# Kernel optimization log

Hardware: AMD Instinct MI355X
Metric: run time of the kernel (lower is better)

The kernel has to match this reference:

```python
import jax, jax.numpy as jnp
import numpy as np
from itertools import permutations

B, Nm, S, K, H, OUT = 32, 128, 16, 4, 128, 1
LG, LI, LGL = 3, 2, 2  # num_layer, num_layer_id, num_layer_global
EPS = 1e-5


def _ln(x, g, b):
    m = jnp.mean(x, -1, keepdims=True)
    v = jnp.mean(jnp.square(x - m), -1, keepdims=True)
    return (x - m) * jax.lax.rsqrt(v + EPS) * g + b


def _block(x, W1, b1, W2, b2, g, bn):
    # Linear -> ReLU -> Linear -> LayerNorm -> ReLU
    h = jax.nn.relu(x @ W1 + b1)
    return jax.nn.relu(_ln(h @ W2 + b2, g, bn))


def setup_inputs() -> dict:
    key = jax.random.key(0)
    ks = iter(jax.random.split(key, 64))
    nrm = lambda shape, s=0.05: jax.random.normal(next(ks), shape, jnp.float32) * s
    x = nrm((B, Nm, 1), 1.0)
    adj = (jax.random.uniform(next(ks), (B, Nm, Nm)) < 0.05).astype(jnp.float32)
    # allperm: all permutations of [1..K-1] with 0 prepended, transposed -> (K, permdim)
    ap = np.array(list(permutations(range(1, K))), dtype=np.int32)
    ap = np.concatenate([np.zeros((ap.shape[0], 1), np.int32), ap], axis=1).T
    allperm = jnp.asarray(ap)
    Ssub = B * S
    base = jax.random.randint(next(ks), (Ssub,), 0, Nm - K)
    subgs = base[:, None] + jnp.arange(K, dtype=jnp.int32)[None, :]  # distinct nodes per subgraph
    num_subg = jnp.full((B,), S, jnp.int32)
    num_node = jnp.full((B,), Nm, jnp.int32)
    d = dict(x=x, adj=adj,
             idemb=nrm((K + 2, H)),
             in_W1=nrm((1, H)), in_b1=jnp.zeros((H,)), in_W2=nrm((H, H)), in_b2=jnp.zeros((H,)),
             in_g=jnp.ones((H,)), in_bn=jnp.zeros((H,)),
             gW1=nrm((LG, H, H)), gb1=jnp.zeros((LG, H)), gW2=nrm((LG, H, H)), gb2=jnp.zeros((LG, H)),
             gg=jnp.ones((LG, H)), gbn=jnp.zeros((LG, H)),
             iW1=nrm((LI, H, H)), ib1=jnp.zeros((LI, H)), iW2=nrm((LI, H, H)), ib2=jnp.zeros((LI, H)),
             ig=jnp.ones((LI, H)), ibn=jnp.zeros((LI, H)),
             glW1=nrm((LGL, H, H)), glb1=jnp.zeros((LGL, H)), glW2=nrm((LGL, H, H)), glb2=jnp.zeros((LGL, H)),
             glg=jnp.ones((LGL, H)), glbn=jnp.zeros((LGL, H)),
             s1_W=nrm((H, H)), s1_b=jnp.zeros((H,)), s2_W=nrm((H, H)), s2_b=jnp.zeros((H,)),
             rW1=nrm((H, H)), rb1=jnp.zeros((H,)), rW2=nrm((H, H)), rb2=jnp.zeros((H,)),
             rg=jnp.ones((H,)), rbn=jnp.zeros((H,)),
             out_W=nrm((H, OUT)), out_b=jnp.zeros((OUT,)),
             subgs=subgs, num_subg=num_subg, num_node=num_node, allperm=allperm)
    return d


def reference(x, adj, idemb, in_W1, in_b1, in_W2, in_b2, in_g, in_bn,
              gW1, gb1, gW2, gb2, gg, gbn,
              iW1, ib1, iW2, ib2, ig, ibn,
              glW1, glb1, glW2, glb2, glg, glbn,
              s1_W, s1_b, s2_W, s2_b,
              rW1, rb1, rW2, rb2, rg, rbn,
              out_W, out_b, subgs, num_subg, num_node, allperm):
    Bsz, N = x.shape[0], x.shape[1]
    Ssub, k = subgs.shape
    permdim = allperm.shape[1]
    # input embedding MLP
    h = _block(x, in_W1, in_b1, in_W2, in_b2, in_g, in_bn)  # (B, Nm, H)
    Hd = h.shape[-1]
    # subgraph -> graph batch map (ns_b = S per graph; Ssub static)
    subgbatch = jnp.repeat(jnp.arange(Bsz), num_subg, total_repeat_length=Ssub)
    # identity labeling: z starts as ones, labeled nodes get idemb(allperm[pos])
    lb = jnp.repeat(jnp.arange(Ssub), k)          # label batch (subgraph idx)
    lnodes = subgs.reshape(-1)                    # node ids within graph
    ni = jnp.tile(jnp.arange(k), Ssub)            # position within subgraph
    vals = idemb[allperm[ni]]                     # (Ssub*k, permdim, H)
    z = jnp.ones((Ssub, N, permdim, Hd), x.dtype)
    z = z.at[lb, lnodes].multiply(vals)
    # graph message passing on full graphs
    for l in range(gW1.shape[0]):
        m = jnp.einsum('bij,bjd->bid', adj, h)
        h = h + _block(m, gW1[l], gb1[l], gW2[l], gb2[l], gg[l], gbn[l])
    hs = h[subgbatch]        # (Ssub, Nm, H)
    sadj = adj[subgbatch]    # (Ssub, Nm, Nm)
    # id message passing over permutation channels
    for l in range(iW1.shape[0]):
        m = jnp.einsum('bij,bjpd->bipd', sadj, z)
        z = z + _block(m, iW1[l], ib1[l], iW2[l], ib2[l], ig[l], ibn[l])
    # zero out padded (null) nodes
    null_mask = jnp.arange(N)[None, :] >= num_node[:, None]  # (B, Nm)
    z = jnp.where(null_mask[subgbatch][:, :, None, None], 0.0, z)
    z = jax.nn.relu(z.mean(axis=2) @ s1_W + s1_b)  # setmlp1, (Ssub, Nm, H)
    hs = hs + z
    for l in range(glW1.shape[0]):
        m = jnp.einsum('bij,bjd->bid', sadj, hs)
        hs = hs + _block(m, glW1[l], glb1[l], glW2[l], glb2[l], glg[l], glbn[l])
    hs = jax.nn.relu(hs.sum(axis=1) @ s2_W + s2_b)  # setmlp2, (Ssub, H)
    pooled = jax.ops.segment_max(hs, subgbatch, num_segments=Bsz)  # global max pool
    pooled = pooled + _block(pooled, rW1, rb1, rW2, rb2, rg, rbn)  # setmlp3 (1 layer)
    return pooled @ out_W + out_b  # (B, OUT)
```

## Files before the change

kernel.cpp:

```cpp
#include <hip/hip_runtime.h>
#include <hip/hip_bf16.h>
#include <string.h>

typedef __hip_bfloat16 bf16;
typedef short v8s __attribute__((ext_vector_type(8)));
typedef float v4f __attribute__((ext_vector_type(4)));

#define H_ 128
#define P_ 6
#define K_ 4

__device__ __forceinline__ float s2f(short s) {
    unsigned int u = ((unsigned int)(unsigned short)s) << 16;
    float f; __builtin_memcpy(&f, &u, 4); return f;
}
__device__ __forceinline__ short f2s(float v) {
    bf16 h = __float2bfloat16(v);
    short s; __builtin_memcpy(&s, &h, 2); return s;
}
__device__ __forceinline__ v4f MFMA(v8s a, v8s b, v4f c) {
    return __builtin_amdgcn_mfma_f32_16x16x32_bf16(a, b, c, 0, 0, 0);
}

__global__ __launch_bounds__(128) void k_deg(const float* __restrict__ adj, float* __restrict__ degf)
{
    __shared__ float red[128];
    const int row = blockIdx.x, t = threadIdx.x;
    red[t] = adj[(size_t)row * 128 + t];
    __syncthreads();
    for (int s = 64; s > 0; s >>= 1) {
        if (t < s) red[t] += red[t + s];
        __syncthreads();
    }
    if (t == 0) degf[row] = red[0];
}

__global__ __launch_bounds__(128) void k_adjb(const float* __restrict__ adj, bf16* __restrict__ adjb)
{
    const size_t i = (size_t)blockIdx.x * 128 + threadIdx.x;
    adjb[i] = __float2bfloat16(adj[i]);
}

__global__ __launch_bounds__(128) void k_wt8(
    const float* s0, const float* s1, const float* s2, const float* s3,
    const float* s4, const float* s5, const float* s6, const float* s7,
    bf16* __restrict__ dst)
{
    const int w = blockIdx.x >> 7, n = blockIdx.x & 127, k = threadIdx.x;
    const float* arr[8] = {s0, s1, s2, s3, s4, s5, s6, s7};
    dst[(size_t)w * 16384 + n * 128 + k] = __float2bfloat16(arr[w][k * 128 + n]);
}

__global__ __launch_bounds__(128) void k_wt1(const float* __restrict__ src, bf16* __restrict__ dst)
{
    const int n = blockIdx.x, k = threadIdx.x;
    dst[n * 128 + k] = __float2bfloat16(src[k * 128 + n]);
}

__global__ __launch_bounds__(256) void k_h_fused(
    const float* __restrict__ x, const bf16* __restrict__ adjb,
    const float* __restrict__ inW1, const float* __restrict__ inb1,
    const bf16* __restrict__ inW2t, const float* __restrict__ inb2,
    const float* __restrict__ ing, const float* __restrict__ inbn,
    const bf16* __restrict__ WTg,
    const float* __restrict__ gb1, const float* __restrict__ gb2,
    const float* __restrict__ gg, const float* __restrict__ gbn,
    float* __restrict__ hb)
{
    __shared__ __align__(16) short sHsT[128][136];
    __shared__ __align__(16) short sM[128][136];
    __shared__ float sP[15][128];
    const int t = threadIdx.x;
    const int g = blockIdx.x;
    const int wave = t >> 6, lane = t & 63, quad = lane >> 4, l16 = lane & 15;
    const int wrow = wave << 5;

    for (int u = t; u < 15 * 128; u += 256) {
        const int a = u >> 7, n = u & 127;
        const float* src;
        if (a == 0) src = inb2;
        else if (a == 1) src = ing;
        else if (a == 2) src = inbn;
        else {
            const int l = (a - 3) >> 2, pp = (a - 3) & 3;
            src = (pp == 0) ? gb1 + l * 128 : (pp == 1) ? gb2 + l * 128
                : (pp == 2) ? gg + l * 128 : gbn + l * 128;
        }
        sP[a][n] = src[n];
    }

    v8s aA[2][4];
    {
        const bf16* ar = adjb + (size_t)g * 16384;
        #pragma unroll
        for (int mt = 0; mt < 2; ++mt)
            #pragma unroll
            for (int kk = 0; kk < 4; ++kk)
                aA[mt][kk] = *(const v8s*)(ar + (size_t)(wrow + mt * 16 + l16) * 128 + kk * 32 + quad * 8);
    }

    {
        const int i = t >> 1, half = (t & 1) * 64;
        const float xv = x[(size_t)g * 128 + i];
        #pragma unroll
        for (int fb = 0; fb < 64; fb += 8) {
            v8s pk;
            #pragma unroll
            for (int e = 0; e < 8; ++e)
                pk[e] = f2s(fmaxf(fmaf(xv, inW1[half + fb + e], inb1[half + fb + e]), 0.f));
            *(v8s*)&sM[i][half + fb] = pk;
        }
    }
    __syncthreads();

    v4f acc[2][8];
    #pragma unroll
    for (int mt = 0; mt < 2; ++mt)
        #pragma unroll
        for (int nt = 0; nt < 8; ++nt) acc[mt][nt] = (v4f){0.f, 0.f, 0.f, 0.f};
    #pragma unroll
    for (int kk = 0; kk < 4; ++kk) {
        v8s a0 = *(const v8s*)&sM[wrow + l16][kk * 32 + quad * 8];
        v8s a1 = *(const v8s*)&sM[wrow + 16 + l16][kk * 32 + quad * 8];
        #pragma unroll
        for (int nt = 0; nt < 8; ++nt) {
            v8s b = *(const v8s*)(inW2t + (nt * 16 + l16) * 128 + kk * 32 + quad * 8);
            acc[0][nt] = MFMA(a0, b, acc[0][nt]);
            acc[1][nt] = MFMA(a1, b, acc[1][nt]);
        }
    }
    float hs_reg[2][8][4];
    #pragma unroll
    for (int mt = 0; mt < 2; ++mt)
        #pragma unroll
        for (int r = 0; r < 4; ++r) {
            float s = 0.f, qq = 0.f;
            #pragma unroll
            for (int nt = 0; nt < 8; ++nt) {
                float u = acc[mt][nt][r] + sP[0][nt * 16 + l16];
                acc[mt][nt][r] = u;
                s += u; qq += u * u;
            }
            #pragma unroll
            for (int d = 1; d < 16; d <<= 1) {
                s += __shfl_xor(s, d);
                qq += __shfl_xor(qq, d);
            }
            float mn = s * (1.f / 128.f);
            float rs = rsqrtf(qq * (1.f / 128.f) - mn * mn + 1e-5f);
            const int i = wrow + mt * 16 + quad * 4 + r;
            #pragma unroll
            for (int nt = 0; nt < 8; ++nt) {
                const int n = nt * 16 + l16;
                float v = fmaxf((acc[mt][nt][r] - mn) * rs * sP[1][n] + sP[2][n], 0.f);
                hs_reg[mt][nt][r] = v;
                sHsT[n][i] = f2s(v);
            }
        }
    __syncthreads();

    for (int l = 0; l < 3; ++l) {
        const bf16* W1t = WTg + (size_t)(2 * l) * 16384;
        const bf16* W2t = WTg + (size_t)(2 * l + 1) * 16384;
        #pragma unroll
        for (int mt = 0; mt < 2; ++mt)
            #pragma unroll
            for (int nt = 0; nt < 8; ++nt) acc[mt][nt] = (v4f){0.f, 0.f, 0.f, 0.f};
        #pragma unroll
        for (int kk = 0; kk < 4; ++kk)
            #pragma unroll
            for (int nt = 0; nt < 8; ++nt) {
                v8s b = *(const v8s*)&sHsT[nt * 16 + l16][kk * 32 + quad * 8];
                acc[0][nt] = MFMA(aA[0][kk], b, acc[0][nt]);
                acc[1][nt] = MFMA(aA[1][kk], b, acc[1][nt]);
            }
        #pragma unroll
        for (int nt = 0; nt < 8; ++nt)
            #pragma unroll
            for (int mt = 0; mt < 2; ++mt)
                #pragma unroll
                for (int r = 0; r < 4; ++r)
                    sM[wrow + mt * 16 + quad * 4 + r][nt * 16 + l16] = f2s(acc[mt][nt][r]);
        __syncthreads();
        #pragma unroll
        for (int mt = 0; mt < 2; ++mt)
            #pragma unroll
            for (int nt = 0; nt < 8; ++nt) acc[mt][nt] = (v4f){0.f, 0.f, 0.f, 0.f};
        #pragma unroll
        for (int kk = 0; kk < 4; ++kk) {
            v8s a0 = *(const v8s*)&sM[wrow + l16][kk * 32 + quad * 8];
            v8s a1 = *(const v8s*)&sM[wrow + 16 + l16][kk * 32 + quad * 8];
            #pragma unroll
            for (int nt = 0; nt < 8; ++nt) {
                v8s b = *(const v8s*)(W1t + (nt * 16 + l16) * 128 + kk * 32 + quad * 8);
                acc[0][nt] = MFMA(a0, b, acc[0][nt]);
                acc[1][nt] = MFMA(a1, b, acc[1][nt]);
            }
        }
        #pragma unroll
        for (int nt = 0; nt < 8; ++nt) {
            float bb = sP[3 + 4 * l + 0][nt * 16 + l16];
            #pragma unroll
            for (int mt = 0; mt < 2; ++mt)
                #pragma unroll
                for (int r = 0; r < 4; ++r)
                    sM[wrow + mt * 16 + quad * 4 + r][nt * 16 + l16] = f2s(fmaxf(acc[mt][nt][r] + bb, 0.f));
        }
        #pragma unroll
        for (int mt = 0; mt < 2; ++mt)
            #pragma unroll
            for (int nt = 0; nt < 8; ++nt) acc[mt][nt] = (v4f){0.f, 0.f, 0.f, 0.f};
        #pragma unroll
        for (int kk = 0; kk < 4; ++kk) {
            v8s a0 = *(const v8s*)&sM[wrow + l16][kk * 32 + quad * 8];
            v8s a1 = *(const v8s*)&sM[wrow + 16 + l16][kk * 32 + quad * 8];
            #pragma unroll
            for (int nt = 0; nt < 8; ++nt) {
                v8s b = *(const v8s*)(W2t + (nt * 16 + l16) * 128 + kk * 32 + quad * 8);
                acc[0][nt] = MFMA(a0, b, acc[0][nt]);
                acc[1][nt] = MFMA(a1, b, acc[1][nt]);
            }
        }
        #pragma unroll
        for (int mt = 0; mt < 2; ++mt)
            #pragma unroll
            for (int r = 0; r < 4; ++r) {
                float s = 0.f, qq = 0.f;
                #pragma unroll
                for (int nt = 0; nt < 8; ++nt) {
                    float u = acc[mt][nt][r] + sP[3 + 4 * l + 1][nt * 16 + l16];
                    acc[mt][nt][r] = u;
                    s += u; qq += u * u;
                }
                #pragma unroll
                for (int d = 1; d < 16; d <<= 1) {
                    s += __shfl_xor(s, d);
                    qq += __shfl_xor(qq, d);
                }
                float mn = s * (1.f / 128.f);
                float rs = rsqrtf(qq * (1.f / 128.f) - mn * mn + 1e-5f);
                const int i = wrow + mt * 16 + quad * 4 + r;
                #pragma unroll
                for (int nt = 0; nt < 8; ++nt) {
                    const int n = nt * 16 + l16;
                    float v = fmaxf((acc[mt][nt][r] - mn) * rs * sP[3 + 4 * l + 2][n] + sP[3 + 4 * l + 3][n], 0.f);
                    float h2 = hs_reg[mt][nt][r] + v;
                    hs_reg[mt][nt][r] = h2;
                    sHsT[n][i] = f2s(h2);
                }
            }
        __syncthreads();
    }

    #pragma unroll
    for (int mt = 0; mt < 2; ++mt)
        #pragma unroll
        for (int nt = 0; nt < 8; ++nt)
            #pragma unroll
            for (int r = 0; r < 4; ++r) {
                const int i = wrow + mt * 16 + quad * 4 + r;
                const int n = nt * 16 + l16;
                hb[((size_t)(g * 128 + i)) * 128 + n] = hs_reg[mt][nt][r];
            }
}

__global__ __launch_bounds__(256) void k_id1_fused(
    const float* __restrict__ adj, const float* __restrict__ degf,
    const int* __restrict__ subgs, const int* __restrict__ allperm,
    const float* __restrict__ idemb, bf16* __restrict__ outb,
    const bf16* __restrict__ W1t, const float* __restrict__ b1,
    const bf16* __restrict__ W2t, const float* __restrict__ b2,
    const float* __restrict__ gam, const float* __restrict__ bet)
{
    __shared__ __align__(16) short sB[128][136];
    __shared__ float sE[K_][128];
    const int t = threadIdx.x;
    const int bi = blockIdx.x;
    const int b_s = bi / 6, p = bi - b_s * 6;
    const int g = b_s >> 4;
    const int wave = t >> 6, lane = t & 63;
    const int quad = lane >> 4, l16 = lane & 15;
    const int wrow = wave << 5;

    int nodeq[K_];
    #pragma unroll
    for (int q = 0; q < K_; ++q) nodeq[q] = subgs[b_s * K_ + q];

    for (int u = t; u < K_ * 128; u += 256) {
        const int q = u >> 7, f = u & 127;
        sE[q][f] = idemb[(size_t)allperm[q * P_ + p] * H_ + f] - 1.f;
    }
    __syncthreads();

    {
        const int i = t >> 1, half = (t & 1) * 64;
        const int gi = g * 128 + i;
        const float dg = degf[gi];
        float aq[K_];
        #pragma unroll
        for (int q = 0; q < K_; ++q) aq[q] = adj[(size_t)gi * 128 + nodeq[q]];
        #pragma unroll
        for (int f = 0; f < 64; ++f) {
            float v = dg;
            #pragma unroll
            for (int q = 0; q < K_; ++q) v = fmaf(aq[q], sE[q][half + f], v);
            sB[i][half + f] = f2s(v);
        }
    }
    __syncthreads();

    v4f acc[2][8];
    #pragma unroll
    for (int mt = 0; mt < 2; ++mt)
        #pragma unroll
        for (int nt = 0; nt < 8; ++nt) acc[mt][nt] = (v4f){0.f, 0.f, 0.f, 0.f};
    #pragma unroll
    for (int kk = 0; kk < 4; ++kk) {
        v8s a0 = *(const v8s*)&sB[wrow + l16][kk * 32 + quad * 8];
        v8s a1 = *(const v8s*)&sB[wrow + 16 + l16][kk * 32 + quad * 8];
        #pragma unroll
        for (int nt = 0; nt < 8; ++nt) {
            v8s b = *(const v8s*)(W1t + (nt * 16 + l16) * 128 + kk * 32 + quad * 8);
            acc[0][nt] = MFMA(a0, b, acc[0][nt]);
            acc[1][nt] = MFMA(a1, b, acc[1][nt]);
        }
    }
    #pragma unroll
    for (int nt = 0; nt < 8; ++nt) {
        float bb = b1[nt * 16 + l16];
        #pragma unroll
        for (int mt = 0; mt < 2; ++mt)
            #pragma unroll
            for (int r = 0; r < 4; ++r)
                sB[wrow + mt * 16 + quad * 4 + r][nt * 16 + l16] = f2s(fmaxf(acc[mt][nt][r] + bb, 0.f));
    }
    #pragma unroll
    for (int mt = 0; mt < 2; ++mt)
        #pragma unroll
        for (int nt = 0; nt < 8; ++nt) acc[mt][nt] = (v4f){0.f, 0.f, 0.f, 0.f};
    #pragma unroll
    for (int kk = 0; kk < 4; ++kk) {
        v8s a0 = *(const v8s*)&sB[wrow + l16][kk * 32 + quad * 8];
        v8s a1 = *(const v8s*)&sB[wrow + 16 + l16][kk * 32 + quad * 8];
        #pragma unroll
        for (int nt = 0; nt < 8; ++nt) {
            v8s b = *(const v8s*)(W2t + (nt * 16 + l16) * 128 + kk * 32 + quad * 8);
            acc[0][nt] = MFMA(a0, b, acc[0][nt]);
            acc[1][nt] = MFMA(a1, b, acc[1][nt]);
        }
    }
    float bb2[8], gv[8], bv[8];
    #pragma unroll
    for (int nt = 0; nt < 8; ++nt) {
        int n = nt * 16 + l16;
        bb2[nt] = b2[n]; gv[nt] = gam[n]; bv[nt] = bet[n];
    }
    #pragma unroll
    for (int mt = 0; mt < 2; ++mt)
        #pragma unroll
        for (int r = 0; r < 4; ++r) {
            float s = 0.f, q = 0.f;
            #pragma unroll
            for (int nt = 0; nt < 8; ++nt) {
                float u = acc[mt][nt][r] + bb2[nt];
                acc[mt][nt][r] = u;
                s += u; q += u * u;
            }
            #pragma unroll
            for (int d = 1; d < 16; d <<= 1) {
                s += __shfl_xor(s, d);
                q += __shfl_xor(q, d);
            }
            float mn = s * (1.f / 128.f);
            float rs = rsqrtf(q * (1.f / 128.f) - mn * mn + 1e-5f);
            #pragma unroll
            for (int nt = 0; nt < 8; ++nt) {
                float v = fmaxf((acc[mt][nt][r] - mn) * rs * gv[nt] + bv[nt], 0.f);
                sB[wrow + mt * 16 + quad * 4 + r][nt * 16 + l16] = f2s(v + 1.0f);
            }
        }
    __syncthreads();
    {
        const int f = t >> 1, nh = (t & 1) * 64;
        const short* flat = &sB[0][0];
        bf16* dst = outb + (size_t)bi * 16384 + (size_t)f * 128 + nh;
        #pragma unroll
        for (int u = 0; u < 8; ++u) {
            v8s pk;
            #pragma unroll
            for (int e = 0; e < 8; ++e) pk[e] = flat[(nh + u * 8 + e) * 136 + f];
            *(v8s*)(dst + u * 8) = pk;
        }
    }
}

__global__ __launch_bounds__(256) void k_id2_v9(
    const bf16* __restrict__ z2t, bf16* __restrict__ zm,
    const bf16* __restrict__ adjb, const int* __restrict__ num_node,
    const int* __restrict__ subgs, const int* __restrict__ allperm,
    const float* __restrict__ idemb,
    const bf16* __restrict__ W1t, const float* __restrict__ b1,
    const bf16* __restrict__ W2t, const float* __restrict__ b2,
    const float* __restrict__ gam, const float* __restrict__ bet)
{
    __shared__ __align__(16) short sB[128][136];
    __shared__ float sP[4][128];
    const int t = threadIdx.x;
    const int b_s = blockIdx.x;
    const int g = b_s >> 4;
    const int wave = t >> 6, lane = t & 63, quad = lane >> 4, l16 = lane & 15;
    const int wrow = wave << 5;

    #pragma unroll
    for (int u = 0; u < 2; ++u) {
        const int v = t + u * 256;
        const int a = v >> 7, n = v & 127;
        const float* src = (a == 0) ? b1 : (a == 1) ? b2 : (a == 2) ? gam : bet;
        sP[a][n] = src[n];
    }

    v8s aA[2][4];
    {
        const bf16* ar = adjb + (size_t)g * 16384;
        #pragma unroll
        for (int mt = 0; mt < 2; ++mt)
            #pragma unroll
            for (int kk = 0; kk < 4; ++kk)
                aA[mt][kk] = *(const v8s*)(ar + (size_t)(wrow + mt * 16 + l16) * 128 + kk * 32 + quad * 8);
    }
    int nodeq[K_];
    #pragma unroll
    for (int q = 0; q < K_; ++q) nodeq[q] = subgs[b_s * K_ + q];

    float macc[2][8][4];
    #pragma unroll
    for (int mt = 0; mt < 2; ++mt)
        #pragma unroll
        for (int nt = 0; nt < 8; ++nt)
            #pragma unroll
            for (int r = 0; r < 4; ++r) macc[mt][nt][r] = 0.f;

    const int sf = t >> 1, shalf = (t & 1) * 64;

    for (int p = 0; p < P_; ++p) {
        {
            const bf16* src = z2t + ((size_t)(b_s * P_ + p)) * 16384 + (size_t)sf * 128 + shalf;
            #pragma unroll
            for (int u = 0; u < 8; ++u)
                *(v8s*)&sB[sf][shalf + u * 8] = *(const v8s*)(src + u * 8);
        }
        __syncthreads();
        if (t < 128) {
            #pragma unroll
            for (int q = 0; q < K_; ++q) {
                float e = idemb[(size_t)allperm[q * P_ + p] * H_ + t] - 1.f;
                short* cell = &sB[t][nodeq[q]];
                *cell = f2s(s2f(*cell) + e);
            }
        }
        __syncthreads();
        #pragma unroll
        for (int mt = 0; mt < 2; ++mt)
            #pragma unroll
            for (int nt = 0; nt < 8; ++nt) {
                const int n = nt * 16 + l16;
                #pragma unroll
                for (int r = 0; r < 4; ++r)
                    macc[mt][nt][r] += s2f(sB[n][wrow + mt * 16 + quad * 4 + r]);
            }
        v4f acc[2][8];
        #pragma unroll
        for (int mt = 0; mt < 2; ++mt)
            #pragma unroll
            for (int nt = 0; nt < 8; ++nt) acc[mt][nt] = (v4f){0.f, 0.f, 0.f, 0.f};
        #pragma unroll
        for (int kk = 0; kk < 4; ++kk)
            #pragma unroll
            for (int nt = 0; nt < 8; ++nt) {
                v8s b = *(const v8s*)&sB[nt * 16 + l16][kk * 32 + quad * 8];
                acc[0][nt] = MFMA(aA[0][kk], b, acc[0][nt]);
                acc[1][nt] = MFMA(aA[1][kk], b, acc[1][nt]);
            }
        __syncthreads();
        #pragma unroll
        for (int nt = 0; nt < 8; ++nt)
            #pragma unroll
            for (int mt = 0; mt < 2; ++mt)
                #pragma unroll
                for (int r = 0; r < 4; ++r)
                    sB[wrow + mt * 16 + quad * 4 + r][nt * 16 + l16] = f2s(acc[mt][nt][r]);
        #pragma unroll
        for (int mt = 0; mt < 2; ++mt)
            #pragma unroll
            for (int nt = 0; nt < 8; ++nt) acc[mt][nt] = (v4f){0.f, 0.f, 0.f, 0.f};
        #pragma unroll
        for (int kk = 0; kk < 4; ++kk) {
            v8s a0 = *(const v8s*)&sB[wrow + l16][kk * 32 + quad * 8];
            v8s a1 = *(const v8s*)&sB[wrow + 16 + l16][kk * 32 + quad * 8];
            #pragma unroll
            for (int nt = 0; nt < 8; ++nt) {
                v8s b = *(const v8s*)(W1t + (nt * 16 + l16) * 128 + kk * 32 + quad * 8);
                acc[0][nt] = MFMA(a0, b, acc[0][nt]);
                acc[1][nt] = MFMA(a1, b, acc[1][nt]);
            }
        }
        #pragma unroll
        for (int nt = 0; nt < 8; ++nt) {
            float bb = sP[0][nt * 16 + l16];
            #pragma unroll
            for (int mt = 0; mt < 2; ++mt)
                #pragma unroll
                for (int r = 0; r < 4; ++r)
                    sB[wrow + mt * 16 + quad * 4 + r][nt * 16 + l16] = f2s(fmaxf(acc[mt][nt][r] + bb, 0.f));
        }
        #pragma unroll
        for (int mt = 0; mt < 2; ++mt)
            #pragma unroll
            for (int nt = 0; nt < 8; ++nt) acc[mt][nt] = (v4f){0.f, 0.f, 0.f, 0.f};
        #pragma unroll
        for (int kk = 0; kk < 4; ++kk) {
            v8s a0 = *(const v8s*)&sB[wrow + l16][kk * 32 + quad * 8];
            v8s a1 = *(const v8s*)&sB[wrow + 16 + l16][kk * 32 + quad * 8];
            #pragma unroll
            for (int nt = 0; nt < 8; ++nt) {
                v8s b = *(const v8s*)(W2t + (nt * 16 + l16) * 128 + kk * 32 + quad * 8);
                acc[0][nt] = MFMA(a0, b, acc[0][nt]);
                acc[1][nt] = MFMA(a1, b, acc[1][nt]);
            }
        }
        #pragma unroll
        for (int mt = 0; mt < 2; ++mt)
            #pragma unroll
            for (int r = 0; r < 4; ++r) {
                float s = 0.f, qq = 0.f;
                #pragma unroll
                for (int nt = 0; nt < 8; ++nt) {
                    float u = acc[mt][nt][r] + sP[1][nt * 16 + l16];
                    acc[mt][nt][r] = u;
                    s += u; qq += u * u;
                }
                #pragma unroll
                for (int d = 1; d < 16; d <<= 1) {
                    s += __shfl_xor(s, d);
                    qq += __shfl_xor(qq, d);
                }
                float mn = s * (1.f / 128.f);
                float rs = rsqrtf(qq * (1.f / 128.f) - mn * mn + 1e-5f);
                #pragma unroll
                for (int nt = 0; nt < 8; ++nt) {
                    const int n = nt * 16 + l16;
                    macc[mt][nt][r] += fmaxf((acc[mt][nt][r] - mn) * rs * sP[2][n] + sP[3][n], 0.f);
                }
            }
        __syncthreads();
    }
    const int nn = num_node[g];
    #pragma unroll
    for (int mt = 0; mt < 2; ++mt)
        #pragma unroll
        for (int nt = 0; nt < 8; ++nt)
            #pragma unroll
            for (int r = 0; r < 4; ++r) {
                const int i = wrow + mt * 16 + quad * 4 + r;
                const int n = nt * 16 + l16;
                float v = (i >= nn) ? 0.f : macc[mt][nt][r] * (1.f / 6.f);
                zm[((size_t)(b_s * 128 + i)) * 128 + n] = __float2bfloat16(v);
            }
}

__global__ __launch_bounds__(256) void k_gl_fused(
    const bf16* __restrict__ zm, const float* __restrict__ hb,
    const bf16* __restrict__ adjb,
    const bf16* __restrict__ s1Wt, const float* __restrict__ s1_b,
    const bf16* __restrict__ WTgl,
    const float* __restrict__ glb1, const float* __restrict__ glb2,
    const float* __restrict__ glg, const float* __restrict__ glbn,
    float* __restrict__ hsum)
{
    __shared__ __align__(16) short sB[128][136];
    __shared__ float sP[9][128];
    const int t = threadIdx.x;
    const int b_s = blockIdx.x;
    const int g = b_s >> 4;
    const int wave = t >> 6, lane = t & 63, quad = lane >> 4, l16 = lane & 15;
    const int wrow = wave << 5;

    for (int u = t; u < 9 * 128; u += 256) {
        const int a = u >> 7, n = u & 127;
        const float* src =
            (a == 0) ? glb1 : (a == 1) ? glb2 : (a == 2) ? glg : (a == 3) ? glbn :
            (a == 4) ? glb1 + 128 : (a == 5) ? glb2 + 128 : (a == 6) ? glg + 128 :
            (a == 7) ? glbn + 128 : s1_b;
        sP[a][n] = src[n];
    }

    v8s aA[2][4];
    {
        const bf16* ar = adjb + (size_t)g * 16384;
        #pragma unroll
        for (int mt = 0; mt < 2; ++mt)
            #pragma unroll
            for (int kk = 0; kk < 4; ++kk)
                aA[mt][kk] = *(const v8s*)(ar + (size_t)(wrow + mt * 16 + l16) * 128 + kk * 32 + quad * 8);
    }

    v4f acc[2][8];
    #pragma unroll
    for (int mt = 0; mt < 2; ++mt)
        #pragma unroll
        for (int nt = 0; nt < 8; ++nt) acc[mt][nt] = (v4f){0.f, 0.f, 0.f, 0.f};
    #pragma unroll
    for (int kk = 0; kk < 4; ++kk) {
        v8s a0 = *(const v8s*)(zm + ((size_t)(b_s * 128) + wrow + l16) * 128 + kk * 32 + quad * 8);
        v8s a1 = *(const v8s*)(zm + ((size_t)(b_s * 128) + wrow + 16 + l16) * 128 + kk * 32 + quad * 8);
        #pragma unroll
        for (int nt = 0; nt < 8; ++nt) {
            v8s b = *(const v8s*)(s1Wt + (nt * 16 + l16) * 128 + kk * 32 + quad * 8);
            acc[0][nt] = MFMA(a0, b, acc[0][nt]);
            acc[1][nt] = MFMA(a1, b, acc[1][nt]);
        }
    }
    __syncthreads();
    float hs_reg[2][8][4];
    #pragma unroll
    for (int mt = 0; mt < 2; ++mt)
        #pragma unroll
        for (int nt = 0; nt < 8; ++nt)
            #pragma unroll
            for (int r = 0; r < 4; ++r) {
                const int i = wrow + mt * 16 + quad * 4 + r;
                const int n = nt * 16 + l16;
                float v = fmaxf(acc[mt][nt][r] + sP[8][n], 0.f);
                v += hb[((size_t)(g * 128 + i)) * 128 + n];
                hs_reg[mt][nt][r] = v;
                sB[n][i] = f2s(v);
            }
    __syncthreads();

    for (int l = 0; l < 2; ++l) {
        const bf16* W1t = WTgl + (size_t)(2 * l) * 16384;
        const bf16* W2t = WTgl + (size_t)(2 * l + 1) * 16384;
        #pragma unroll
        for (int mt = 0; mt < 2; ++mt)
            #pragma unroll
            for (int nt = 0; nt < 8; ++nt) acc[mt][nt] = (v4f){0.f, 0.f, 0.f, 0.f};
        #pragma unroll
        for (int kk = 0; kk < 4; ++kk)
            #pragma unroll
            for (int nt = 0; nt < 8; ++nt) {
                v8s b = *(const v8s*)&sB[nt * 16 + l16][kk * 32 + quad * 8];
                acc[0][nt] = MFMA(aA[0][kk], b, acc[0][nt]);
                acc[1][nt] = MFMA(aA[1][kk], b, acc[1][nt]);
            }
        __syncthreads();
        #pragma unroll
        for (int nt = 0; nt < 8; ++nt)
            #pragma unroll
            for (int mt = 0; mt < 2; ++mt)
                #pragma unroll
                for (int r = 0; r < 4; ++r)
                    sB[wrow + mt * 16 + quad * 4 + r][nt * 16 + l16] = f2s(acc[mt][nt][r]);
        #pragma unroll
        for (int mt = 0; mt < 2; ++mt)
            #pragma unroll
            for (int nt = 0; nt < 8; ++nt) acc[mt][nt] = (v4f){0.f, 0.f, 0.f, 0.f};
        #pragma unroll
        for (int kk = 0; kk < 4; ++kk) {
            v8s a0 = *(const v8s*)&sB[wrow + l16][kk * 32 + quad * 8];
            v8s a1 = *(const v8s*)&sB[wrow + 16 + l16][kk * 32 + quad * 8];
            #pragma unroll
            for (int nt = 0; nt < 8; ++nt) {
                v8s b = *(const v8s*)(W1t + (nt * 16 + l16) * 128 + kk * 32 + quad * 8);
                acc[0][nt] = MFMA(a0, b, acc[0][nt]);
                acc[1][nt] = MFMA(a1, b, acc[1][nt]);
            }
        }
        #pragma unroll
        for (int nt = 0; nt < 8; ++nt) {
            float bb = sP[4 * l + 0][nt * 16 + l16];
            #pragma unroll
            for (int mt = 0; mt < 2; ++mt)
                #pragma unroll
                for (int r = 0; r < 4; ++r)
                    sB[wrow + mt * 16 + quad * 4 + r][nt * 16 + l16] = f2s(fmaxf(acc[mt][nt][r] + bb, 0.f));
        }
        #pragma unroll
        for (int mt = 0; mt < 2; ++mt)
            #pragma unroll
            for (int nt = 0; nt < 8; ++nt) acc[mt][nt] = (v4f){0.f, 0.f, 0.f, 0.f};
        #pragma unroll
        for (int kk = 0; kk < 4; ++kk) {
            v8s a0 = *(const v8s*)&sB[wrow + l16][kk * 32 + quad * 8];
            v8s a1 = *(const v8s*)&sB[wrow + 16 + l16][kk * 32 + quad * 8];
            #pragma unroll
            for (int nt = 0; nt < 8; ++nt) {
                v8s b = *(const v8s*)(W2t + (nt * 16 + l16) * 128 + kk * 32 + quad * 8);
                acc[0][nt] = MFMA(a0, b, acc[0][nt]);
                acc[1][nt] = MFMA(a1, b, acc[1][nt]);
            }
        }
        __syncthreads();
        #pragma unroll
        for (int mt = 0; mt < 2; ++mt)
            #pragma unroll
            for (int r = 0; r < 4; ++r) {
                float s = 0.f, qq = 0.f;
                #pragma unroll
                for (int nt = 0; nt < 8; ++nt) {
                    float u = acc[mt][nt][r] + sP[4 * l + 1][nt * 16 + l16];
                    acc[mt][nt][r] = u;
                    s += u; qq += u * u;
                }
                #pragma unroll
                for (int d = 1; d < 16; d <<= 1) {
                    s += __shfl_xor(s, d);
                    qq += __shfl_xor(qq, d);
                }
                float mn = s * (1.f / 128.f);
                float rs = rsqrtf(qq * (1.f / 128.f) - mn * mn + 1e-5f);
                const int i = wrow + mt * 16 + quad * 4 + r;
                #pragma unroll
                for (int nt = 0; nt < 8; ++nt) {
                    const int n = nt * 16 + l16;
                    float v = fmaxf((acc[mt][nt][r] - mn) * rs * sP[4 * l + 2][n] + sP[4 * l + 3][n], 0.f);
                    float h2 = hs_reg[mt][nt][r] + v;
                    hs_reg[mt][nt][r] = h2;
                    sB[n][i] = f2s(h2);
                }
            }
        __syncthreads();
    }

    float* sRedf = (float*)&sB[0][0];
    #pragma unroll
    for (int nt = 0; nt < 8; ++nt) {
        float part = 0.f;
        #pragma unroll
        for (int mt = 0; mt < 2; ++mt)
            #pragma unroll
            for (int r = 0; r < 4; ++r) part += hs_reg[mt][nt][r];
        sRedf[(wave * 4 + quad) * 128 + nt * 16 + l16] = part;
    }
    __syncthreads();
    if (t < 128) {
        float s = 0.f;
        #pragma unroll
        for (int r = 0; r < 16; ++r) s += sRedf[r * 128 + t];
        hsum[(size_t)b_s * 128 + t] = s;
    }
}

__global__ __launch_bounds__(128) void k_tail(const float* __restrict__ hsum,
    const float* __restrict__ s2W, const float* __restrict__ s2b,
    const float* __restrict__ rW1, const float* __restrict__ rb1,
    const float* __restrict__ rW2, const float* __restrict__ rb2,
    const float* __restrict__ rg, const float* __restrict__ rbn,
    const float* __restrict__ outW, const float* __restrict__ outb,
    float* __restrict__ out)
{
    __shared__ float sA[16][136];
    __shared__ float sV[128];
    __shared__ float red[128];
    const int g = blockIdx.x, hd = threadIdx.x;
    #pragma unroll
    for (int r = 0; r < 16; ++r) sA[r][hd] = hsum[((size_t)(g * 16 + r)) * 128 + hd];
    __syncthreads();
    float acc[16];
    #pragma unroll
    for (int r = 0; r < 16; ++r) acc[r] = s2b[hd];
    for (int k = 0; k < 128; k += 4) {
        float w0 = s2W[(k+0)*128+hd], w1 = s2W[(k+1)*128+hd], w2 = s2W[(k+2)*128+hd], w3 = s2W[(k+3)*128+hd];
        #pragma unroll
        for (int r = 0; r < 16; ++r) {
            float4 a = *(const float4*)&sA[r][k];
            acc[r] = fmaf(a.x, w0, acc[r]); acc[r] = fmaf(a.y, w1, acc[r]);
            acc[r] = fmaf(a.z, w2, acc[r]); acc[r] = fmaf(a.w, w3, acc[r]);
        }
    }
    float pool = 0.f;
    pool = -INFINITY;
    #pragma unroll
    for (int r = 0; r < 16; ++r) pool = fmaxf(pool, fmaxf(acc[r], 0.f));
    sV[hd] = pool;
    __syncthreads();
    float t1 = rb1[hd];
    for (int k = 0; k < 128; ++k) t1 = fmaf(sV[k], rW1[k * 128 + hd], t1);
    t1 = fmaxf(t1, 0.f);
    red[hd] = t1;
    __syncthreads();
    float u = rb2[hd];
    for (int k = 0; k < 128; ++k) u = fmaf(red[k], rW2[k * 128 + hd], u);
    float* rs1 = (float*)&sA[0][0];
    float* rs2 = (float*)&sA[2][0];
    rs1[hd] = u; rs2[hd] = u * u;
    __syncthreads();
    for (int s = 64; s > 0; s >>= 1) {
        if (hd < s) { rs1[hd] += rs1[hd + s]; rs2[hd] += rs2[hd + s]; }
        __syncthreads();
    }
    float mn = rs1[0] * (1.f / 128.f);
    float var = rs2[0] * (1.f / 128.f) - mn * mn;
    float rstd = rsqrtf(var + 1e-5f);
    float p2 = fmaxf((u - mn) * rstd * rg[hd] + rbn[hd], 0.f) + sV[hd];
    __syncthreads();
    red[hd] = p2 * outW[hd];
    __syncthreads();
    for (int s = 64; s > 0; s >>= 1) {
        if (hd < s) red[hd] += red[hd + s];
        __syncthreads();
    }
    if (hd == 0) out[g] = red[0] + outb[0];
}

extern "C" void kernel_launch(void* const* d_in, const int* in_sizes, int n_in,
                              void* d_out, int out_size, void* d_ws, size_t ws_size,
                              hipStream_t stream)
{
    (void)in_sizes; (void)n_in; (void)out_size; (void)ws_size;
    const float* x     = (const float*)d_in[0];
    const float* adj   = (const float*)d_in[1];
    const float* idemb = (const float*)d_in[2];
    const float* in_W1 = (const float*)d_in[3];
    const float* in_b1 = (const float*)d_in[4];
    const float* in_W2 = (const float*)d_in[5];
    const float* in_b2 = (const float*)d_in[6];
    const float* in_g  = (const float*)d_in[7];
    const float* in_bn = (const float*)d_in[8];
    const float* gW1   = (const float*)d_in[9];
    const float* gb1   = (const float*)d_in[10];
    const float* gW2   = (const float*)d_in[11];
    const float* gb2   = (const float*)d_in[12];
    const float* gg    = (const float*)d_in[13];
    const float* gbn   = (const float*)d_in[14];
    const float* iW1   = (const float*)d_in[15];
    const float* ib1   = (const float*)d_in[16];
    const float* iW2   = (const float*)d_in[17];
    const float* ib2   = (const float*)d_in[18];
    const float* ig    = (const float*)d_in[19];
    const float* ibn   = (const float*)d_in[20];
    const float* glW1  = (const float*)d_in[21];
    const float* glb1  = (const float*)d_in[22];
    const float* glW2  = (const float*)d_in[23];
    const float* glb2  = (const float*)d_in[24];
    const float* glg   = (const float*)d_in[25];
    const float* glbn  = (const float*)d_in[26];
    const float* s1_W  = (const float*)d_in[27];
    const float* s1_b  = (const float*)d_in[28];
    const float* s2_W  = (const float*)d_in[29];
    const float* s2_b  = (const float*)d_in[30];
    const float* rW1   = (const float*)d_in[31];
    const float* rb1   = (const float*)d_in[32];
    const float* rW2   = (const float*)d_in[33];
    const float* rb2   = (const float*)d_in[34];
    const float* rg    = (const float*)d_in[35];
    const float* rbn   = (const float*)d_in[36];
    const float* out_W = (const float*)d_in[37];
    const float* out_b = (const float*)d_in[38];
    const int* subgs   = (const int*)d_in[39];
    const int* num_node= (const int*)d_in[41];
    const int* allperm = (const int*)d_in[42];

    const size_t MB_ = (size_t)512 * 128 * P_ * H_ * 2;
    char* w = (char*)d_ws;
    bf16*  mz     = (bf16*)(w);
    bf16*  s1Wt   = (bf16*)(w + 33554432ull);
    bf16*  zm     = (bf16*)(w + MB_);
    bf16*  WT     = (bf16*)(w + MB_ + 16777216ull);
    char*  wc     = w + MB_ + 16777216ull + 262144ull;
    float* hb     = (float*)(wc);
    bf16*  adjb   = (bf16*)(wc + 2097152ull);
    bf16*  WT2    = (bf16*)(wc + 3145728ull);
    float* hsum   = (float*)(wc + 4194304ull);
    float* degf   = (float*)(wc + 4964352ull);
    float* outp   = (float*)d_out;

    k_deg<<<4096, 128, 0, stream>>>(adj, degf);
    k_wt8<<<1024, 128, 0, stream>>>(iW1, iW2, iW1 + 16384, iW2 + 16384,
                                    glW1, glW2, glW1 + 16384, glW2 + 16384, WT);
    k_wt8<<<1024, 128, 0, stream>>>(in_W2, gW1, gW2, gW1 + 16384,
                                    gW2 + 16384, gW1 + 32768, gW2 + 32768, in_W2, WT2);
    k_adjb<<<4096, 128, 0, stream>>>(adj, adjb);

    k_h_fused<<<32, 256, 0, stream>>>(x, adjb, in_W1, in_b1,
        WT2, in_b2, in_g, in_bn,
        WT2 + 16384, gb1, gb2, gg, gbn, hb);

    k_id1_fused<<<3072, 256, 0, stream>>>(adj, degf, subgs, allperm, idemb, mz,
        WT, ib1, WT + 16384, ib2, ig, ibn);

    k_id2_v9<<<512, 256, 0, stream>>>(mz, zm, adjb, num_node, subgs, allperm, idemb,
        WT + 2 * 16384, ib1 + 128, WT + 3 * 16384, ib2 + 128, ig + 128, ibn + 128);

    k_wt1<<<128, 128, 0, stream>>>(s1_W, s1Wt);

    k_gl_fused<<<512, 256, 0, stream>>>(zm, hb, adjb, s1Wt, s1_b,
        WT + 4 * 16384, glb1, glb2, glg, glbn, hsum);

    k_tail<<<32, 128, 0, stream>>>(hsum, s2_W, s2_b, rW1, rb1, rW2, rb2,
        rg, rbn, out_W, out_b, outp);
}
```

Measured before the change: 564.9 us.

## Merge prep kernels and fuse id1 with h-path into one launch

```diff
diff --git a/kernel.cpp b/kernel.cpp
--- a/kernel.cpp
+++ b/kernel.cpp
@@ -22,42 +22,49 @@
     return __builtin_amdgcn_mfma_f32_16x16x32_bf16(a, b, c, 0, 0, 0);
 }
 
-__global__ __launch_bounds__(128) void k_deg(const float* __restrict__ adj, float* __restrict__ degf)
+__global__ __launch_bounds__(128) void k_prep(const float* __restrict__ adj,
+    float* __restrict__ degf, bf16* __restrict__ adjb,
+    const float* __restrict__ iW1, const float* __restrict__ iW2,
+    const float* __restrict__ glW1, const float* __restrict__ glW2,
+    const float* __restrict__ in_W2, const float* __restrict__ gW1,
+    const float* __restrict__ gW2, const float* __restrict__ s1_W,
+    bf16* __restrict__ WT, bf16* __restrict__ WT2, bf16* __restrict__ s1Wt)
 {
     __shared__ float red[128];
-    const int row = blockIdx.x, t = threadIdx.x;
-    red[t] = adj[(size_t)row * 128 + t];
-    __syncthreads();
-    for (int s = 64; s > 0; s >>= 1) {
-        if (t < s) red[t] += red[t + s];
-        __syncthreads();
-    }
-    if (t == 0) degf[row] = red[0];
+    const int b = blockIdx.x, t = threadIdx.x;
+    if (b < 4096) {
+        float a = adj[(size_t)b * 128 + t];
+        adjb[(size_t)b * 128 + t] = __float2bfloat16(a);
+        red[t] = a;
+        __syncthreads();
+        for (int s = 64; s > 0; s >>= 1) {
+            if (t < s) red[t] += red[t + s];
+            __syncthreads();
+        }
+        if (t == 0) degf[b] = red[0];
+    } else if (b < 5120) {
+        const int bb = b - 4096, w = bb >> 7, n = bb & 127;
+        const float* arr[8] = {iW1, iW2, iW1 + 16384, iW2 + 16384,
+                               glW1, glW2, glW1 + 16384, glW2 + 16384};
+        WT[(size_t)w * 16384 + n * 128 + t] = __float2bfloat16(arr[w][t * 128 + n]);
+    } else if (b < 6144) {
+        const int bb = b - 5120, w = bb >> 7, n = bb & 127;
+        const float* arr[8] = {in_W2, gW1, gW2, gW1 + 16384,
+                               gW2 + 16384, gW1 + 32768, gW2 + 32768, in_W2};
+        WT2[(size_t)w * 16384 + n * 128 + t] = __float2bfloat16(arr[w][t * 128 + n]);
+    } else {
+        const int n = b - 6144;
+        s1Wt[n * 128 + t] = __float2bfloat16(s1_W[t * 128 + n]);
+    }
 }
 
-__global__ __launch_bounds__(128) void k_adjb(const float* __restrict__ adj, bf16* __restrict__ adjb)
-{
-    const size_t i = (size_t)blockIdx.x * 128 + threadIdx.x;
-    adjb[i] = __float2bfloat16(adj[i]);
-}
-
-__global__ __launch_bounds__(128) void k_wt8(
-    const float* s0, const float* s1, const float* s2, const float* s3,
-    const float* s4, const float* s5, const float* s6, const float* s7,
-    bf16* __restrict__ dst)
-{
-    const int w = blockIdx.x >> 7, n = blockIdx.x & 127, k = threadIdx.x;
-    const float* arr[8] = {s0, s1, s2, s3, s4, s5, s6, s7};
-    dst[(size_t)w * 16384 + n * 128 + k] = __float2bfloat16(arr[w][k * 128 + n]);
-}
-
-__global__ __launch_bounds__(128) void k_wt1(const float* __restrict__ src, bf16* __restrict__ dst)
-{
-    const int n = blockIdx.x, k = threadIdx.x;
-    dst[n * 128 + k] = __float2bfloat16(src[k * 128 + n]);
-}
-
-__global__ __launch_bounds__(256) void k_h_fused(
+__global__ __launch_bounds__(256) void k_id1h(
+    const float* __restrict__ adj, const float* __restrict__ degf,
+    const int* __restrict__ subgs, const int* __restrict__ allperm,
+    const float* __restrict__ idemb, bf16* __restrict__ outb,
+    const bf16* __restrict__ W1t, const float* __restrict__ b1,
+    const bf16* __restrict__ W2t, const float* __restrict__ b2,
+    const float* __restrict__ gam, const float* __restrict__ bet,
     const float* __restrict__ x, const bf16* __restrict__ adjb,
     const float* __restrict__ inW1, const float* __restrict__ inb1,
     const bf16* __restrict__ inW2t, const float* __restrict__ inb2,
@@ -67,13 +74,132 @@
     const float* __restrict__ gg, const float* __restrict__ gbn,
     float* __restrict__ hb)
 {
-    __shared__ __align__(16) short sHsT[128][136];
-    __shared__ __align__(16) short sM[128][136];
+    __shared__ __align__(16) short sB[128][136];
     __shared__ float sP[15][128];
     const int t = threadIdx.x;
-    const int g = blockIdx.x;
     const int wave = t >> 6, lane = t & 63, quad = lane >> 4, l16 = lane & 15;
     const int wrow = wave << 5;
+
+    if (blockIdx.x < 3072) {
+        const int bi = blockIdx.x;
+        const int b_s = bi / 6, p = bi - b_s * 6;
+        const int g = b_s >> 4;
+        float (*sE)[128] = sP;
+
+        int nodeq[K_];
+        #pragma unroll
+        for (int q = 0; q < K_; ++q) nodeq[q] = subgs[b_s * K_ + q];
+
+        for (int u = t; u < K_ * 128; u += 256) {
+            const int q = u >> 7, f = u & 127;
+            sE[q][f] = idemb[(size_t)allperm[q * P_ + p] * H_ + f] - 1.f;
+        }
+        __syncthreads();
+
+        {
+            const int i = t >> 1, half = (t & 1) * 64;
+            const int gi = g * 128 + i;
+            const float dg = degf[gi];
+            float aq[K_];
+            #pragma unroll
+            for (int q = 0; q < K_; ++q) aq[q] = adj[(size_t)gi * 128 + nodeq[q]];
+            #pragma unroll
+            for (int f = 0; f < 64; ++f) {
+                float v = dg;
+                #pragma unroll
+                for (int q = 0; q < K_; ++q) v = fmaf(aq[q], sE[q][half + f], v);
+                sB[i][half + f] = f2s(v);
+            }
+        }
+        __syncthreads();
+
+        v4f acc[2][8];
+        #pragma unroll
+        for (int mt = 0; mt < 2; ++mt)
+            #pragma unroll
+            for (int nt = 0; nt < 8; ++nt) acc[mt][nt] = (v4f){0.f, 0.f, 0.f, 0.f};
+        #pragma unroll
+        for (int kk = 0; kk < 4; ++kk) {
+            v8s a0 = *(const v8s*)&sB[wrow + l16][kk * 32 + quad * 8];
+            v8s a1 = *(const v8s*)&sB[wrow + 16 + l16][kk * 32 + quad * 8];
+            #pragma unroll
+            for (int nt = 0; nt < 8; ++nt) {
+                v8s b = *(const v8s*)(W1t + (nt * 16 + l16) * 128 + kk * 32 + quad * 8);
+                acc[0][nt] = MFMA(a0, b, acc[0][nt]);
+                acc[1][nt] = MFMA(a1, b, acc[1][nt]);
+            }
+        }
+        #pragma unroll
+        for (int nt = 0; nt < 8; ++nt) {
+            float bb = b1[nt * 16 + l16];
+            #pragma unroll
+            for (int mt = 0; mt < 2; ++mt)
+                #pragma unroll
+                for (int r = 0; r < 4; ++r)
+                    sB[wrow + mt * 16 + quad * 4 + r][nt * 16 + l16] = f2s(fmaxf(acc[mt][nt][r] + bb, 0.f));
+        }
+        #pragma unroll
+        for (int mt = 0; mt < 2; ++mt)
+            #pragma unroll
+            for (int nt = 0; nt < 8; ++nt) acc[mt][nt] = (v4f){0.f, 0.f, 0.f, 0.f};
+        #pragma unroll
+        for (int kk = 0; kk < 4; ++kk) {
+            v8s a0 = *(const v8s*)&sB[wrow + l16][kk * 32 + quad * 8];
+            v8s a1 = *(const v8s*)&sB[wrow + 16 + l16][kk * 32 + quad * 8];
+            #pragma unroll
+            for (int nt = 0; nt < 8; ++nt) {
+                v8s b = *(const v8s*)(W2t + (nt * 16 + l16) * 128 + kk * 32 + quad * 8);
+                acc[0][nt] = MFMA(a0, b, acc[0][nt]);
+                acc[1][nt] = MFMA(a1, b, acc[1][nt]);
+            }
+        }
+        float bb2[8], gv[8], bv[8];
+        #pragma unroll
+        for (int nt = 0; nt < 8; ++nt) {
+            int n = nt * 16 + l16;
+            bb2[nt] = b2[n]; gv[nt] = gam[n]; bv[nt] = bet[n];
+        }
+        #pragma unroll
+        for (int mt = 0; mt < 2; ++mt)
+            #pragma unroll
+            for (int r = 0; r < 4; ++r) {
+                float s = 0.f, q = 0.f;
+                #pragma unroll
+                for (int nt = 0; nt < 8; ++nt) {
+                    float u = acc[mt][nt][r] + bb2[nt];
+                    acc[mt][nt][r] = u;
+                    s += u; q += u * u;
+                }
+                #pragma unroll
+                for (int d = 1; d < 16; d <<= 1) {
+                    s += __shfl_xor(s, d);
+                    q += __shfl_xor(q, d);
+                }
+                float mn = s * (1.f / 128.f);
+                float rs = rsqrtf(q * (1.f / 128.f) - mn * mn + 1e-5f);
+                #pragma unroll
+                for (int nt = 0; nt < 8; ++nt) {
+                    float v = fmaxf((acc[mt][nt][r] - mn) * rs * gv[nt] + bv[nt], 0.f);
+                    sB[wrow + mt * 16 + quad * 4 + r][nt * 16 + l16] = f2s(v + 1.0f);
+                }
+            }
+        __syncthreads();
+        {
+            const int f = t >> 1, nh = (t & 1) * 64;
+            const short* flat = &sB[0][0];
+            bf16* dst = outb + (size_t)bi * 16384 + (size_t)f * 128 + nh;
+            #pragma unroll
+            for (int u = 0; u < 8; ++u) {
+                v8s pk;
+                #pragma unroll
+                for (int e = 0; e < 8; ++e) pk[e] = flat[(nh + u * 8 + e) * 136 + f];
+                *(v8s*)(dst + u * 8) = pk;
+            }
+        }
+        return;
+    }
+
+    const int g = blockIdx.x - 3072;
 
     for (int u = t; u < 15 * 128; u += 256) {
         const int a = u >> 7, n = u & 127;
@@ -108,11 +234,9 @@
             #pragma unroll
             for (int e = 0; e < 8; ++e)
                 pk[e] = f2s(fmaxf(fmaf(xv, inW1[half + fb + e], inb1[half + fb + e]), 0.f));
-            *(v8s*)&sM[i][half + fb] = pk;
-        }
-    }
-    __syncthreads();
-
+            *(v8s*)&sB[i][half + fb] = pk;
+        }
+    }
     v4f acc[2][8];
     #pragma unroll
     for (int mt = 0; mt < 2; ++mt)
@@ -120,8 +244,8 @@
         for (int nt = 0; nt < 8; ++nt) acc[mt][nt] = (v4f){0.f, 0.f, 0.f, 0.f};
     #pragma unroll
     for (int kk = 0; kk < 4; ++kk) {
-        v8s a0 = *(const v8s*)&sM[wrow + l16][kk * 32 + quad * 8];
-        v8s a1 = *(const v8s*)&sM[wrow + 16 + l16][kk * 32 + quad * 8];
+        v8s a0 = *(const v8s*)&sB[wrow + l16][kk * 32 + quad * 8];
+        v8s a1 = *(const v8s*)&sB[wrow + 16 + l16][kk * 32 + quad * 8];
         #pragma unroll
         for (int nt = 0; nt < 8; ++nt) {
             v8s b = *(const v8s*)(inW2t + (nt * 16 + l16) * 128 + kk * 32 + quad * 8);
@@ -129,6 +253,7 @@
             acc[1][nt] = MFMA(a1, b, acc[1][nt]);
         }
     }
+    __syncthreads();
     float hs_reg[2][8][4];
     #pragma unroll
     for (int mt = 0; mt < 2; ++mt)
@@ -154,14 +279,14 @@
                 const int n = nt * 16 + l16;
                 float v = fmaxf((acc[mt][nt][r] - mn) * rs * sP[1][n] + sP[2][n], 0.f);
                 hs_reg[mt][nt][r] = v;
-                sHsT[n][i] = f2s(v);
+                sB[n][i] = f2s(v);
             }
         }
     __syncthreads();
 
     for (int l = 0; l < 3; ++l) {
-        const bf16* W1t = WTg + (size_t)(2 * l) * 16384;
-        const bf16* W2t = WTg + (size_t)(2 * l + 1) * 16384;
+        const bf16* W1t_ = WTg + (size_t)(2 * l) * 16384;
+        const bf16* W2t_ = WTg + (size_t)(2 * l + 1) * 16384;
         #pragma unroll
         for (int mt = 0; mt < 2; ++mt)
             #pragma unroll
@@ -170,29 +295,29 @@
         for (int kk = 0; kk < 4; ++kk)
             #pragma unroll
             for (int nt = 0; nt < 8; ++nt) {
-                v8s b = *(const v8s*)&sHsT[nt * 16 + l16][kk * 32 + quad * 8];
+                v8s b = *(const v8s*)&sB[nt * 16 + l16][kk * 32 + quad * 8];
                 acc[0][nt] = MFMA(aA[0][kk], b, acc[0][nt]);
                 acc[1][nt] = MFMA(aA[1][kk], b, acc[1][nt]);
             }
+        __syncthreads();
         #pragma unroll
         for (int nt = 0; nt < 8; ++nt)
             #pragma unroll
             for (int mt = 0; mt < 2; ++mt)
                 #pragma unroll
                 for (int r = 0; r < 4; ++r)
-                    sM[wrow + mt * 16 + quad * 4 + r][nt * 16 + l16] = f2s(acc[mt][nt][r]);
-        __syncthreads();
+                    sB[wrow + mt * 16 + quad * 4 + r][nt * 16 + l16] = f2s(acc[mt][nt][r]);
         #pragma unroll
         for (int mt = 0; mt < 2; ++mt)
             #pragma unroll
             for (int nt = 0; nt < 8; ++nt) acc[mt][nt] = (v4f){0.f, 0.f, 0.f, 0.f};
         #pragma unroll
         for (int kk = 0; kk < 4; ++kk) {
-            v8s a0 = *(const v8s*)&sM[wrow + l16][kk * 32 + quad * 8];
-            v8s a1 = *(const v8s*)&sM[wrow + 16 + l16][kk * 32 + quad * 8];
-            #pragma unroll
-            for (int nt = 0; nt < 8; ++nt) {
-                v8s b = *(const v8s*)(W1t + (nt * 16 + l16) * 128 + kk * 32 + quad * 8);
+            v8s a0 = *(const v8s*)&sB[wrow + l16][kk * 32 + quad * 8];
+            v8s a1 = *(const v8s*)&sB[wrow + 16 + l16][kk * 32 + quad * 8];
+            #pragma unroll
+            for (int nt = 0; nt < 8; ++nt) {
+                v8s b = *(const v8s*)(W1t_ + (nt * 16 + l16) * 128 + kk * 32 + quad * 8);
                 acc[0][nt] = MFMA(a0, b, acc[0][nt]);
                 acc[1][nt] = MFMA(a1, b, acc[1][nt]);
             }
@@ -204,7 +329,7 @@
             for (int mt = 0; mt < 2; ++mt)
                 #pragma unroll
                 for (int r = 0; r < 4; ++r)
-                    sM[wrow + mt * 16 + quad * 4 + r][nt * 16 + l16] = f2s(fmaxf(acc[mt][nt][r] + bb, 0.f));
+                    sB[wrow + mt * 16 + quad * 4 + r][nt * 16 + l16] = f2s(fmaxf(acc[mt][nt][r] + bb, 0.f));
         }
         #pragma unroll
         for (int mt = 0; mt < 2; ++mt)
@@ -212,15 +337,16 @@
             for (int nt = 0; nt < 8; ++nt) acc[mt][nt] = (v4f){0.f, 0.f, 0.f, 0.f};
         #pragma unroll
         for (int kk = 0; kk < 4; ++kk) {
-            v8s a0 = *(const v8s*)&sM[wrow + l16][kk * 32 + quad * 8];
-            v8s a1 = *(const v8s*)&sM[wrow + 16 + l16][kk * 32 + quad * 8];
-            #pragma unroll
-            for (int nt = 0; nt < 8; ++nt) {
-                v8s b = *(const v8s*)(W2t + (nt * 16 + l16) * 128 + kk * 32 + quad * 8);
+            v8s a0 = *(const v8s*)&sB[wrow + l16][kk * 32 + quad * 8];
+            v8s a1 = *(const v8s*)&sB[wrow + 16 + l16][kk * 32 + quad * 8];
+            #pragma unroll
+            for (int nt = 0; nt < 8; ++nt) {
+                v8s b = *(const v8s*)(W2t_ + (nt * 16 + l16) * 128 + kk * 32 + quad * 8);
                 acc[0][nt] = MFMA(a0, b, acc[0][nt]);
                 acc[1][nt] = MFMA(a1, b, acc[1][nt]);
             }
         }
+        __syncthreads();
         #pragma unroll
         for (int mt = 0; mt < 2; ++mt)
             #pragma unroll
@@ -246,7 +372,7 @@
                     float v = fmaxf((acc[mt][nt][r] - mn) * rs * sP[3 + 4 * l + 2][n] + sP[3 + 4 * l + 3][n], 0.f);
                     float h2 = hs_reg[mt][nt][r] + v;
                     hs_reg[mt][nt][r] = h2;
-                    sHsT[n][i] = f2s(h2);
+                    sB[n][i] = f2s(h2);
                 }
             }
         __syncthreads();
@@ -262,136 +388,6 @@
                 const int n = nt * 16 + l16;
                 hb[((size_t)(g * 128 + i)) * 128 + n] = hs_reg[mt][nt][r];
             }
-}
-
-__global__ __launch_bounds__(256) void k_id1_fused(
-    const float* __restrict__ adj, const float* __restrict__ degf,
-    const int* __restrict__ subgs, const int* __restrict__ allperm,
-    const float* __restrict__ idemb, bf16* __restrict__ outb,
-    const bf16* __restrict__ W1t, const float* __restrict__ b1,
-    const bf16* __restrict__ W2t, const float* __restrict__ b2,
-    const float* __restrict__ gam, const float* __restrict__ bet)
-{
-    __shared__ __align__(16) short sB[128][136];
-    __shared__ float sE[K_][128];
-    const int t = threadIdx.x;
-    const int bi = blockIdx.x;
-    const int b_s = bi / 6, p = bi - b_s * 6;
-    const int g = b_s >> 4;
-    const int wave = t >> 6, lane = t & 63;
-    const int quad = lane >> 4, l16 = lane & 15;
-    const int wrow = wave << 5;
-
-    int nodeq[K_];
-    #pragma unroll
-    for (int q = 0; q < K_; ++q) nodeq[q] = subgs[b_s * K_ + q];
-
-    for (int u = t; u < K_ * 128; u += 256) {
-        const int q = u >> 7, f = u & 127;
-        sE[q][f] = idemb[(size_t)allperm[q * P_ + p] * H_ + f] - 1.f;
-    }
-    __syncthreads();
-
-    {
-        const int i = t >> 1, half = (t & 1) * 64;
-        const int gi = g * 128 + i;
-        const float dg = degf[gi];
-        float aq[K_];
-        #pragma unroll
-        for (int q = 0; q < K_; ++q) aq[q] = adj[(size_t)gi * 128 + nodeq[q]];
-        #pragma unroll
-        for (int f = 0; f < 64; ++f) {
-            float v = dg;
-            #pragma unroll
-            for (int q = 0; q < K_; ++q) v = fmaf(aq[q], sE[q][half + f], v);
-            sB[i][half + f] = f2s(v);
-        }
-    }
-    __syncthreads();
-
-    v4f acc[2][8];
-    #pragma unroll
-    for (int mt = 0; mt < 2; ++mt)
-        #pragma unroll
-        for (int nt = 0; nt < 8; ++nt) acc[mt][nt] = (v4f){0.f, 0.f, 0.f, 0.f};
-    #pragma unroll
-    for (int kk = 0; kk < 4; ++kk) {
-        v8s a0 = *(const v8s*)&sB[wrow + l16][kk * 32 + quad * 8];
-        v8s a1 = *(const v8s*)&sB[wrow + 16 + l16][kk * 32 + quad * 8];
-        #pragma unroll
-        for (int nt = 0; nt < 8; ++nt) {
-            v8s b = *(const v8s*)(W1t + (nt * 16 + l16) * 128 + kk * 32 + quad * 8);
-            acc[0][nt] = MFMA(a0, b, acc[0][nt]);
-            acc[1][nt] = MFMA(a1, b, acc[1][nt]);
-        }
-    }
-    #pragma unroll
-    for (int nt = 0; nt < 8; ++nt) {
-        float bb = b1[nt * 16 + l16];
-        #pragma unroll
-        for (int mt = 0; mt < 2; ++mt)
-            #pragma unroll
-            for (int r = 0; r < 4; ++r)
-                sB[wrow + mt * 16 + quad * 4 + r][nt * 16 + l16] = f2s(fmaxf(acc[mt][nt][r] + bb, 0.f));
-    }
-    #pragma unroll
-    for (int mt = 0; mt < 2; ++mt)
-        #pragma unroll
-        for (int nt = 0; nt < 8; ++nt) acc[mt][nt] = (v4f){0.f, 0.f, 0.f, 0.f};
-    #pragma unroll
-    for (int kk = 0; kk < 4; ++kk) {
-        v8s a0 = *(const v8s*)&sB[wrow + l16][kk * 32 + quad * 8];
-        v8s a1 = *(const v8s*)&sB[wrow + 16 + l16][kk * 32 + quad * 8];
-        #pragma unroll
-        for (int nt = 0; nt < 8; ++nt) {
-            v8s b = *(const v8s*)(W2t + (nt * 16 + l16) * 128 + kk * 32 + quad * 8);
-            acc[0][nt] = MFMA(a0, b, acc[0][nt]);
-            acc[1][nt] = MFMA(a1, b, acc[1][nt]);
-        }
-    }
-    float bb2[8], gv[8], bv[8];
-    #pragma unroll
-    for (int nt = 0; nt < 8; ++nt) {
-        int n = nt * 16 + l16;
-        bb2[nt] = b2[n]; gv[nt] = gam[n]; bv[nt] = bet[n];
-    }
-    #pragma unroll
-    for (int mt = 0; mt < 2; ++mt)
-        #pragma unroll
-        for (int r = 0; r < 4; ++r) {
-            float s = 0.f, q = 0.f;
-            #pragma unroll
-            for (int nt = 0; nt < 8; ++nt) {
-                float u = acc[mt][nt][r] + bb2[nt];
-                acc[mt][nt][r] = u;
-                s += u; q += u * u;
-            }
-            #pragma unroll
-            for (int d = 1; d < 16; d <<= 1) {
-                s += __shfl_xor(s, d);
-                q += __shfl_xor(q, d);
-            }
-            float mn = s * (1.f / 128.f);
-            float rs = rsqrtf(q * (1.f / 128.f) - mn * mn + 1e-5f);
-            #pragma unroll
-            for (int nt = 0; nt < 8; ++nt) {
-                float v = fmaxf((acc[mt][nt][r] - mn) * rs * gv[nt] + bv[nt], 0.f);
-                sB[wrow + mt * 16 + quad * 4 + r][nt * 16 + l16] = f2s(v + 1.0f);
-            }
-        }
-    __syncthreads();
-    {
-        const int f = t >> 1, nh = (t & 1) * 64;
-        const short* flat = &sB[0][0];
-        bf16* dst = outb + (size_t)bi * 16384 + (size_t)f * 128 + nh;
-        #pragma unroll
-        for (int u = 0; u < 8; ++u) {
-            v8s pk;
-            #pragma unroll
-            for (int e = 0; e < 8; ++e) pk[e] = flat[(nh + u * 8 + e) * 136 + f];
-            *(v8s*)(dst + u * 8) = pk;
-        }
-    }
 }
 
 __global__ __launch_bounds__(256) void k_id2_v9(
@@ -777,8 +773,7 @@
             acc[r] = fmaf(a.z, w2, acc[r]); acc[r] = fmaf(a.w, w3, acc[r]);
         }
     }
-    float pool = 0.f;
-    pool = -INFINITY;
+    float pool = -INFINITY;
     #pragma unroll
     for (int r = 0; r < 16; ++r) pool = fmaxf(pool, fmaxf(acc[r], 0.f));
     sV[hd] = pool;
@@ -871,29 +866,26 @@
     bf16*  adjb   = (bf16*)(wc + 2097152ull);
     bf16*  WT2    = (bf16*)(wc + 3145728ull);
     float* hsum   = (float*)(wc + 4194304ull);
+    bf16*  s1WtX  = (bf16*)(wc + 4456448ull);
     float* degf   = (float*)(wc + 4964352ull);
     float* outp   = (float*)d_out;
-
-    k_deg<<<4096, 128, 0, stream>>>(adj, degf);
-    k_wt8<<<1024, 128, 0, stream>>>(iW1, iW2, iW1 + 16384, iW2 + 16384,
-                                    glW1, glW2, glW1 + 16384, glW2 + 16384, WT);
-    k_wt8<<<1024, 128, 0, stream>>>(in_W2, gW1, gW2, gW1 + 16384,
-                                    gW2 + 16384, gW1 + 32768, gW2 + 32768, in_W2, WT2);
-    k_adjb<<<4096, 128, 0, stream>>>(adj, adjb);
-
-    k_h_fused<<<32, 256, 0, stream>>>(x, adjb, in_W1, in_b1,
+    (void)s1Wt;
+
+    k_prep<<<6272, 128, 0, stream>>>(adj, degf, adjb,
+        iW1, iW2, glW1, glW2, in_W2, gW1, gW2, s1_W,
+        WT, WT2, s1WtX);
+
+    k_id1h<<<3104, 256, 0, stream>>>(
+        adj, degf, subgs, allperm, idemb, mz,
+        WT, ib1, WT + 16384, ib2, ig, ibn,
+        x, adjb, in_W1, in_b1,
         WT2, in_b2, in_g, in_bn,
         WT2 + 16384, gb1, gb2, gg, gbn, hb);
 
-    k_id1_fused<<<3072, 256, 0, stream>>>(adj, degf, subgs, allperm, idemb, mz,
-        WT, ib1, WT + 16384, ib2, ig, ibn);
-
     k_id2_v9<<<512, 256, 0, stream>>>(mz, zm, adjb, num_node, subgs, allperm, idemb,
         WT + 2 * 16384, ib1 + 128, WT + 3 * 16384, ib2 + 128, ig + 128, ibn + 128);
 
-    k_wt1<<<128, 128, 0, stream>>>(s1_W, s1Wt);
-
-    k_gl_fused<<<512, 256, 0, stream>>>(zm, hb, adjb, s1Wt, s1_b,
+    k_gl_fused<<<512, 256, 0, stream>>>(zm, hb, adjb, s1WtX, s1_b,
         WT + 4 * 16384, glb1, glb2, glg, glbn, hsum);
 
     k_tail<<<32, 128, 0, stream>>>(hsum, s2_W, s2_b, rW1, rb1, rW2, rb2,
```

Measured after the change: 611.2 us. 1.08x slower.
